# Kernel tuning notes

Measured on AMD Instinct MI355X. Metric: run time of the kernel, lower is better.

Reference implementation:

```python
import jax, jax.numpy as jnp
import numpy as np
import math

NUM_HEADS = 16
D_MODEL = 1024
D_HEAD = D_MODEL // NUM_HEADS
B, S = 2, 2048


def setup_inputs() -> dict:
    key = jax.random.key(0)
    k1, k2 = jax.random.split(key)
    query = jax.random.normal(k1, (B, S, D_MODEL), dtype=jnp.float32)
    # causal mask: True where masked (j > i)
    mask = jnp.broadcast_to(jnp.triu(jnp.ones((S, S), dtype=bool), k=1), (B, S, S))
    W_o = jax.random.normal(k2, (D_MODEL, D_MODEL), dtype=jnp.float32) * (1.0 / math.sqrt(D_MODEL))
    b_o = jnp.zeros((D_MODEL,), dtype=jnp.float32)
    return {"query": query, "mask": mask, "W_o": W_o, "b_o": b_o}


def reference(query, mask, W_o, b_o):
    # NOTE: faithful to source — q/k/v linear layers are never applied in forward.
    # Self-attention: key = value = query.
    Bq, Sq, D = query.shape
    # split heads: [B, S, D] -> [B, H, S, dh]
    q = query.reshape(Bq, Sq, NUM_HEADS, D_HEAD).transpose(0, 2, 1, 3)
    k = q
    v = q
    # logits: [B, H, Sq, Sk]
    logits = jnp.einsum("bhqd,bhkd->bhqk", q, k) / math.sqrt(D_HEAD)
    logits = jnp.where(mask[:, None, :, :], -jnp.inf, logits)
    attn = jax.nn.softmax(logits, axis=-1)          # [B, H, Sq, Sk]
    out = jnp.einsum("bhqk,bhkd->bhqd", attn, v)    # [B, H, Sq, dh]
    # merge heads: [B, Sq, D]
    out = out.transpose(0, 2, 1, 3).reshape(Bq, Sq, D)
    # output projection (torch Linear: x @ W.T + b)
    return out @ W_o.T + b_o
```

## Files before the change

### kernel.cpp

```cpp
#include <hip/hip_runtime.h>
#include <hip/hip_bf16.h>
#include <stdint.h>

#define SEQ 2048
#define DMODEL 1024

typedef __attribute__((ext_vector_type(8))) short short8;
typedef __attribute__((ext_vector_type(4))) float floatx4;

__device__ __forceinline__ floatx4 mfma16x16x32(short8 a, short8 b, floatx4 c) {
  return __builtin_amdgcn_mfma_f32_16x16x32_bf16(a, b, c, 0, 0, 0);
}

__device__ __forceinline__ uint16_t f2bf(float x) {
  __hip_bfloat16 h = __float2bfloat16(x);
  return *reinterpret_cast<uint16_t*>(&h);
}

__device__ __forceinline__ void glds16(const uint16_t* g, uint16_t* l) {
  __builtin_amdgcn_global_load_lds(
      (const __attribute__((address_space(1))) uint32_t*)g,
      (__attribute__((address_space(3))) uint32_t*)(uint32_t)(uintptr_t)l,
      16, 0, 0);
}

__global__ __launch_bounds__(256) void cvt_kernel(
    const float* __restrict__ q, uint16_t* __restrict__ qd,
    const float* __restrict__ w, uint16_t* __restrict__ wd,
    int nq4, int ntot4) {
  int i = blockIdx.x * 256 + threadIdx.x;
  if (i >= ntot4) return;
  const float* src = (i < nq4) ? q : w;
  uint16_t* dst = (i < nq4) ? qd : wd;
  int j = (i < nq4) ? i : i - nq4;
  float4 v = ((const float4*)src)[j];
  ushort4 r;
  r.x = f2bf(v.x); r.y = f2bf(v.y); r.z = f2bf(v.z); r.w = f2bf(v.w);
  ((ushort4*)dst)[j] = r;
}

__device__ __forceinline__ int vt_idx(int d, int key) {
  return d * 64 + ((((key >> 3) ^ (d >> 3) ^ d) & 7) << 3) + (key & 7);
}

__device__ __forceinline__ int ps_idx(int row, int col) {
  return row * 64 + ((((col >> 3) ^ row) & 7) << 3) + (col & 7);
}

__global__ __launch_bounds__(256, 2) void attn_kernel(
    const uint16_t* __restrict__ qbf, uint16_t* __restrict__ xout) {
  const int g  = blockIdx.x >> 5;
  const int qt = (g < 8) ? 15 - g : g - 8;
  const int bh = blockIdx.x & 31;
  const int b  = bh >> 4;
  const int h  = bh & 15;
  const int tid  = threadIdx.x;
  const int wave = tid >> 6;
  const int lane = tid & 63;
  const int l15  = lane & 15;
  const int quad = lane >> 4;

  __shared__ uint16_t Vt[2][64 * 64];
  __shared__ uint16_t Ps[4][2][16 * 64];

  const uint16_t* base = qbf + (size_t)b * SEQ * DMODEL + h * 64;

  short8 qf[2][2];
  #pragma unroll
  for (int s = 0; s < 2; ++s)
    #pragma unroll
    for (int ks = 0; ks < 2; ++ks)
      qf[s][ks] = *(const short8*)(base +
          (size_t)(qt * 128 + s * 64 + wave * 16 + l15) * DMODEL + ks * 32 + quad * 8);

  floatx4 o_acc[2][4];
  float l_run[2][4];
  #pragma unroll
  for (int s = 0; s < 2; ++s) {
    #pragma unroll
    for (int dt = 0; dt < 4; ++dt) o_acc[s][dt] = (floatx4){0.f, 0.f, 0.f, 0.f};
    #pragma unroll
    for (int r = 0; r < 4; ++r) l_run[s][r] = 0.f;
  }

  const int r0 = tid >> 3;
  const int cg = (tid & 7) * 8;

  auto stage = [&](int kt, int buf) {
    uint4 v0 = *(const uint4*)(base + (size_t)(kt * 64 + r0) * DMODEL + cg);
    uint4 v1 = *(const uint4*)(base + (size_t)(kt * 64 + 32 + r0) * DMODEL + cg);
    uint16_t t0[8], t1[8];
    *(uint4*)t0 = v0;
    *(uint4*)t1 = v1;
    #pragma unroll
    for (int i = 0; i < 8; ++i) Vt[buf][vt_idx(cg + i, r0)] = t0[i];
    #pragma unroll
    for (int i = 0; i < 8; ++i) Vt[buf][vt_idx(cg + i, 32 + r0)] = t1[i];
  };

  const int ktmax = 2 * qt + 1;
  stage(0, 0);

  auto iter = [&](int kt, int nt0, int nt1, bool d0, bool d1, int ks0m, int ks1m) {
    __syncthreads();
    if (kt < ktmax) stage(kt + 1, (kt + 1) & 1);
    const int buf = kt & 1;

    floatx4 sacc[2][4];
    #pragma unroll
    for (int s = 0; s < 2; ++s)
      #pragma unroll
      for (int nt = 0; nt < 4; ++nt) sacc[s][nt] = (floatx4){0.f, 0.f, 0.f, 0.f};

    #pragma unroll
    for (int ks = 0; ks < 2; ++ks)
      #pragma unroll
      for (int nt = 0; nt < 4; ++nt) {
        short8 kf = *(const short8*)(base +
            (size_t)(kt * 64 + nt * 16 + l15) * DMODEL + ks * 32 + quad * 8);
        if (nt <= nt0) sacc[0][nt] = mfma16x16x32(qf[0][ks], kf, sacc[0][nt]);
        if (nt <= nt1) sacc[1][nt] = mfma16x16x32(qf[1][ks], kf, sacc[1][nt]);
      }

    #pragma unroll
    for (int s = 0; s < 2; ++s) {
      const int ntm = s ? nt1 : nt0;
      const bool dg = s ? d1 : d0;
      const int ksm = s ? ks1m : ks0m;
      if (ntm < 0) continue;
      uint16_t* Pw = Ps[wave][s];
      #pragma unroll
      for (int nt = 0; nt < 4; ++nt) {
        const int lcol = nt * 16 + l15;
        if (nt <= ntm) {
          #pragma unroll
          for (int r = 0; r < 4; ++r) {
            float p = __builtin_amdgcn_exp2f(fmaf(sacc[s][nt][r], 0.1803369f, -10.f));
            if (dg && nt == wave && l15 > quad * 4 + r) p = 0.f;
            l_run[s][r] += p;
            Pw[ps_idx(quad * 4 + r, lcol)] = f2bf(p);
          }
        } else if (nt <= 2 * ksm + 1) {
          #pragma unroll
          for (int r = 0; r < 4; ++r) Pw[ps_idx(quad * 4 + r, lcol)] = 0;
        }
      }
      #pragma unroll
      for (int ks = 0; ks < 2; ++ks)
        if (ks <= ksm) {
          short8 pf = *(const short8*)&Pw[ps_idx(l15, ks * 32 + quad * 8)];
          #pragma unroll
          for (int dt = 0; dt < 4; ++dt) {
            short8 vf = *(const short8*)&Vt[buf][vt_idx(dt * 16 + l15, ks * 32 + quad * 8)];
            o_acc[s][dt] = mfma16x16x32(pf, vf, o_acc[s][dt]);
          }
        }
    }
  };

  const int kdiag = (wave < 2) ? 0 : 1;
  for (int kt = 0; kt < ktmax - 1; ++kt)
    iter(kt, 3, 3, false, false, 1, 1);
  iter(ktmax - 1, wave, 3, true, false, kdiag, 1);
  iter(ktmax, -1, wave, false, true, 0, kdiag);

  #pragma unroll
  for (int s = 0; s < 2; ++s)
    #pragma unroll
    for (int r = 0; r < 4; ++r) {
      float l = l_run[s][r];
      #pragma unroll
      for (int off = 1; off < 16; off <<= 1) l += __shfl_xor(l, off, 64);
      float inv = 1.0f / l;
      int rowg = b * SEQ + qt * 128 + s * 64 + wave * 16 + quad * 4 + r;
      #pragma unroll
      for (int dt = 0; dt < 4; ++dt)
        xout[(size_t)rowg * DMODEL + h * 64 + dt * 16 + l15] =
            f2bf(o_acc[s][dt][r] * inv);
    }
}

__global__ __launch_bounds__(256, 4) void proj_kernel(
    const uint16_t* __restrict__ X, const uint16_t* __restrict__ Wo,
    const float* __restrict__ bo, float* __restrict__ out) {
  const int bx = blockIdx.x;
  const int by = blockIdx.y;
  const int tid = threadIdx.x;
  const int wave = tid >> 6, lane = tid & 63, l15 = lane & 15, quad = lane >> 4;
  const int wr = wave >> 1, wc = wave & 1;

  __shared__ uint16_t As[2][128 * 32];
  __shared__ uint16_t Bs[2][64 * 32];

  floatx4 acc[4][2];
  #pragma unroll
  for (int mt = 0; mt < 4; ++mt)
    #pragma unroll
    for (int nt = 0; nt < 2; ++nt) acc[mt][nt] = (floatx4){0.f, 0.f, 0.f, 0.f};

  const int rw = lane >> 2;
  const int kp = 8 * ((lane & 3) ^ ((lane >> 2) & 3));

  auto stage = [&](int kt, int buf) {
    glds16(X + (size_t)(bx * 128 + wave * 16 + rw) * DMODEL + kt * 32 + kp,
           &As[buf][(wave * 16) * 32 + lane * 8]);
    glds16(X + (size_t)(bx * 128 + 64 + wave * 16 + rw) * DMODEL + kt * 32 + kp,
           &As[buf][(64 + wave * 16) * 32 + lane * 8]);
    glds16(Wo + (size_t)(by * 64 + wave * 16 + rw) * DMODEL + kt * 32 + kp,
           &Bs[buf][(wave * 16) * 32 + lane * 8]);
  };

  stage(0, 0);
  for (int kt = 0; kt < 32; ++kt) {
    __syncthreads();
    if (kt < 31) stage(kt + 1, (kt + 1) & 1);
    const int buf = kt & 1;
    short8 af[4], bf2[2];
    #pragma unroll
    for (int mt = 0; mt < 4; ++mt) {
      int row = wr * 64 + mt * 16 + l15;
      af[mt] = *(const short8*)&As[buf][row * 32 + ((quad ^ (row & 3)) << 3)];
    }
    #pragma unroll
    for (int nt = 0; nt < 2; ++nt) {
      int row = wc * 32 + nt * 16 + l15;
      bf2[nt] = *(const short8*)&Bs[buf][row * 32 + ((quad ^ (row & 3)) << 3)];
    }
    #pragma unroll
    for (int mt = 0; mt < 4; ++mt)
      #pragma unroll
      for (int nt = 0; nt < 2; ++nt)
        acc[mt][nt] = mfma16x16x32(af[mt], bf2[nt], acc[mt][nt]);
  }

  #pragma unroll
  for (int nt = 0; nt < 2; ++nt) {
    int colg = by * 64 + wc * 32 + nt * 16 + l15;
    float bias = bo[colg];
    #pragma unroll
    for (int mt = 0; mt < 4; ++mt)
      #pragma unroll
      for (int r2 = 0; r2 < 4; ++r2) {
        int rowg = bx * 128 + wr * 64 + mt * 16 + quad * 4 + r2;
        out[(size_t)rowg * DMODEL + colg] = acc[mt][nt][r2] + bias;
      }
  }
}

extern "C" void kernel_launch(void* const* d_in, const int* in_sizes, int n_in,
                              void* d_out, int out_size, void* d_ws, size_t ws_size,
                              hipStream_t stream) {
  const float* q_f32  = (const float*)d_in[0];
  const float* Wo_f32 = (const float*)d_in[2];
  const float* bo     = (const float*)d_in[3];
  float* out = (float*)d_out;

  uint16_t* qbf  = (uint16_t*)d_ws;
  uint16_t* X    = (uint16_t*)((char*)d_ws + (size_t)8 * 1024 * 1024);
  uint16_t* wobf = (uint16_t*)((char*)d_ws + (size_t)16 * 1024 * 1024);

  const int nq4 = 2 * SEQ * DMODEL / 4;
  const int nw4 = DMODEL * DMODEL / 4;
  const int nt4 = nq4 + nw4;
  cvt_kernel<<<dim3((nt4 + 255) / 256), dim3(256), 0, stream>>>(
      q_f32, qbf, Wo_f32, wobf, nq4, nt4);

  attn_kernel<<<dim3(512), dim3(256), 0, stream>>>(qbf, X);
  proj_kernel<<<dim3(32, 16), dim3(256), 0, stream>>>(X, wobf, bo, out);
}
```

Measured before the change: 163.6 us.

## Split attention key range across two blocks per query tile, then combine partials

Each query tile's causal key range is split into two halves handled by separate blocks, doubling the grid to 1024 blocks and raising the launch-bounds occupancy hint to 4 blocks per CU. The aim is to shorten the longest blocks and even out the causal work across CUs. Each block writes unnormalized bf16 partial outputs and row sums, and a new combine kernel adds the two halves and normalizes. The cost is an extra kernel launch and extra global traffic for the partials. It also adds bf16 rounding on the unnormalized sums, and the combine is only correct if both halves share the same softmax max offset.

Measured after the change: 291.6 us. 1.78x slower.

```diff
diff --git a/kernel.cpp b/kernel.cpp
--- a/kernel.cpp
+++ b/kernel.cpp
@@ -15,6 +15,11 @@
 __device__ __forceinline__ uint16_t f2bf(float x) {
   __hip_bfloat16 h = __float2bfloat16(x);
   return *reinterpret_cast<uint16_t*>(&h);
+}
+
+__device__ __forceinline__ float bf2f(uint16_t u) {
+  uint32_t x = (uint32_t)u << 16;
+  union { uint32_t u; float f; } c; c.u = x; return c.f;
 }
 
 __device__ __forceinline__ void glds16(const uint16_t* g, uint16_t* l) {
@@ -47,13 +52,15 @@
   return row * 64 + ((((col >> 3) ^ row) & 7) << 3) + (col & 7);
 }
 
-__global__ __launch_bounds__(256, 2) void attn_kernel(
-    const uint16_t* __restrict__ qbf, uint16_t* __restrict__ xout) {
-  const int g  = blockIdx.x >> 5;
-  const int qt = (g < 8) ? 15 - g : g - 8;
-  const int bh = blockIdx.x & 31;
-  const int b  = bh >> 4;
-  const int h  = bh & 15;
+__global__ __launch_bounds__(256, 4) void attn_kernel(
+    const uint16_t* __restrict__ qbf, uint16_t* __restrict__ Opart,
+    float* __restrict__ Lpart) {
+  const int w    = blockIdx.x >> 5;
+  const int qt   = 15 - (w >> 1);
+  const int half = w & 1;
+  const int bh   = blockIdx.x & 31;
+  const int b    = bh >> 4;
+  const int h    = bh & 15;
   const int tid  = threadIdx.x;
   const int wave = tid >> 6;
   const int lane = tid & 63;
@@ -98,12 +105,13 @@
     for (int i = 0; i < 8; ++i) Vt[buf][vt_idx(cg + i, 32 + r0)] = t1[i];
   };
 
-  const int ktmax = 2 * qt + 1;
-  stage(0, 0);
+  const int ktlo = half ? (qt + 1) : 0;
+  const int kthi = half ? (2 * qt + 1) : qt;
+  stage(ktlo, ktlo & 1);
 
   auto iter = [&](int kt, int nt0, int nt1, bool d0, bool d1, int ks0m, int ks1m) {
     __syncthreads();
-    if (kt < ktmax) stage(kt + 1, (kt + 1) & 1);
+    if (kt < kthi) stage(kt + 1, (kt + 1) & 1);
     const int buf = kt & 1;
 
     floatx4 sacc[2][4];
@@ -159,11 +167,19 @@
   };
 
   const int kdiag = (wave < 2) ? 0 : 1;
-  for (int kt = 0; kt < ktmax - 1; ++kt)
-    iter(kt, 3, 3, false, false, 1, 1);
-  iter(ktmax - 1, wave, 3, true, false, kdiag, 1);
-  iter(ktmax, -1, wave, false, true, 0, kdiag);
-
+  if (half == 0) {
+    if (qt == 0) {
+      iter(0, wave, 3, true, false, kdiag, 1);
+    } else {
+      for (int kt = 0; kt <= qt; ++kt) iter(kt, 3, 3, false, false, 1, 1);
+    }
+  } else {
+    for (int kt = qt + 1; kt < 2 * qt; ++kt) iter(kt, 3, 3, false, false, 1, 1);
+    if (qt >= 1) iter(2 * qt, wave, 3, true, false, kdiag, 1);
+    iter(2 * qt + 1, -1, wave, false, true, 0, kdiag);
+  }
+
+  const size_t obase = (size_t)half * (4096 * 1024);
   #pragma unroll
   for (int s = 0; s < 2; ++s)
     #pragma unroll
@@ -171,13 +187,30 @@
       float l = l_run[s][r];
       #pragma unroll
       for (int off = 1; off < 16; off <<= 1) l += __shfl_xor(l, off, 64);
-      float inv = 1.0f / l;
       int rowg = b * SEQ + qt * 128 + s * 64 + wave * 16 + quad * 4 + r;
+      if (l15 == 0) Lpart[half * 65536 + h * 4096 + rowg] = l;
       #pragma unroll
       for (int dt = 0; dt < 4; ++dt)
-        xout[(size_t)rowg * DMODEL + h * 64 + dt * 16 + l15] =
-            f2bf(o_acc[s][dt][r] * inv);
-    }
+        Opart[obase + (size_t)rowg * DMODEL + h * 64 + dt * 16 + l15] =
+            f2bf(o_acc[s][dt][r]);
+    }
+}
+
+__global__ __launch_bounds__(256) void combine_kernel(
+    const uint16_t* __restrict__ Opart, const float* __restrict__ Lpart,
+    uint16_t* __restrict__ X) {
+  int i = blockIdx.x * 256 + threadIdx.x;
+  int row = i >> 7;
+  int c8  = (i & 127) * 8;
+  int h   = c8 >> 6;
+  float inv = 1.0f / (Lpart[h * 4096 + row] + Lpart[65536 + h * 4096 + row]);
+  uint16_t a[8], bpt[8], o[8];
+  *(uint4*)a   = *(const uint4*)&Opart[(size_t)row * DMODEL + c8];
+  *(uint4*)bpt = *(const uint4*)&Opart[(size_t)4096 * 1024 + (size_t)row * DMODEL + c8];
+  #pragma unroll
+  for (int k = 0; k < 8; ++k)
+    o[k] = f2bf((bf2f(a[k]) + bf2f(bpt[k])) * inv);
+  *(uint4*)&X[(size_t)row * DMODEL + c8] = *(uint4*)o;
 }
 
 __global__ __launch_bounds__(256, 4) void proj_kernel(
@@ -255,9 +288,11 @@
   const float* bo     = (const float*)d_in[3];
   float* out = (float*)d_out;
 
-  uint16_t* qbf  = (uint16_t*)d_ws;
-  uint16_t* X    = (uint16_t*)((char*)d_ws + (size_t)8 * 1024 * 1024);
-  uint16_t* wobf = (uint16_t*)((char*)d_ws + (size_t)16 * 1024 * 1024);
+  uint16_t* qbf   = (uint16_t*)d_ws;
+  uint16_t* X     = (uint16_t*)((char*)d_ws + (size_t)8 * 1024 * 1024);
+  uint16_t* wobf  = (uint16_t*)((char*)d_ws + (size_t)16 * 1024 * 1024);
+  uint16_t* Opart = (uint16_t*)((char*)d_ws + (size_t)18 * 1024 * 1024);
+  float*    Lpart = (float*)((char*)d_ws + (size_t)34 * 1024 * 1024);
 
   const int nq4 = 2 * SEQ * DMODEL / 4;
   const int nw4 = DMODEL * DMODEL / 4;
@@ -265,6 +300,7 @@
   cvt_kernel<<<dim3((nt4 + 255) / 256), dim3(256), 0, stream>>>(
       q_f32, qbf, Wo_f32, wobf, nq4, nt4);
 
-  attn_kernel<<<dim3(512), dim3(256), 0, stream>>>(qbf, X);
+  attn_kernel<<<dim3(1024), dim3(256), 0, stream>>>(qbf, Opart, Lpart);
+  combine_kernel<<<dim3(2048), dim3(256), 0, stream>>>(Opart, Lpart, X);
   proj_kernel<<<dim3(32, 16), dim3(256), 0, stream>>>(X, wobf, bo, out);
 }
```
